# Kernel optimization log

Measured on AMD Instinct MI355X. Metric: run time of the kernel, lower is better.

## Reference

```python
import jax, jax.numpy as jnp
import numpy as np

TIMESTEPS = 1000
NOISE_LEVEL = 0.1


def setup_inputs() -> dict:
    key = jax.random.key(0)
    # images normalized to [0, 1], matching the clip range used by the model
    x = jax.random.uniform(key, (32, 512, 512, 3), dtype=jnp.float32)
    return {"x": x}


def reference(x):
    # --- forward diffusion: 1000 truly sequential add-noise + clip steps ---
    fwd_keys = jax.random.split(jax.random.key(1), TIMESTEPS)

    def fwd_step(img, k):
        noise = NOISE_LEVEL * jax.random.normal(k, img.shape, dtype=img.dtype)
        return jnp.clip(img + noise, 0.0, 1.0), None

    noisy, _ = jax.lax.scan(fwd_step, x, fwd_keys)

    # --- reverse diffusion ---
    # In the original code the reverse loop recomputes `denoised_image` from the
    # UNCHANGED `noisy_image` every iteration, so only the final iteration's
    # random draw determines the output. Mathematically equivalent single step:
    rev_key = jax.random.fold_in(jax.random.key(2), TIMESTEPS - 1)
    rev_noise = NOISE_LEVEL * jax.random.normal(rev_key, noisy.shape, dtype=noisy.dtype)
    out = jnp.clip(noisy - rev_noise, 0.0, 1.0)
    return out
```

## Files before the change

kernel.cpp:

```cpp
#include <hip/hip_runtime.h>
#include <stdint.h>


#define NTOTAL 25165824u
#define EPT    8u
#define NTHREADS (NTOTAL / EPT)
#define TS     1000

__device__ __forceinline__ void tf2x32(uint32_t k0, uint32_t k1,
                                       uint32_t x0, uint32_t x1,
                                       uint32_t& o0, uint32_t& o1) {
  const uint32_t k2 = k0 ^ k1 ^ 0x1BD11BDAu;
  x0 += k0; x1 += k1;
#define RR(r) { x0 += x1; x1 = (x1 << (r)) | (x1 >> (32 - (r))); x1 ^= x0; }
  RR(13) RR(15) RR(26) RR(6)
  x0 += k1; x1 += k2 + 1u;
  RR(17) RR(29) RR(16) RR(24)
  x0 += k2; x1 += k0 + 2u;
  RR(13) RR(15) RR(26) RR(6)
  x0 += k0; x1 += k1 + 3u;
  RR(17) RR(29) RR(16) RR(24)
  x0 += k1; x1 += k2 + 4u;
  RR(13) RR(15) RR(26) RR(6)
  x0 += k2; x1 += k0 + 5u;
#undef RR
  o0 = x0; o1 = x1;
}

__device__ __forceinline__ uint32_t tf_bits(uint32_t k0, uint32_t k1, uint32_t i) {
  uint32_t o0, o1;
  tf2x32(k0, k1, 0u, i, o0, o1);
  return o0 ^ o1;
}

__device__ __forceinline__ float bits_to_u(uint32_t b) {
  float f = __uint_as_float((b >> 9) | 0x3f800000u) - 1.0f;
  float u = fmaf(f, 2.0f, -0.99999994f);
  return fmaxf(-0.99999994f, u);
}

__device__ __forceinline__ float erfinv_f(float x) {
#pragma clang fp contract(off)
  float t = x * x;
  float m = -t;
  float u = m + 1.0f;
  float lg;
  if (u == 1.0f) {
    lg = m;
  } else {
    lg = m * __fdividef(__logf(u), u - 1.0f);
  }
  float w = -lg;
  float p;
  if (w < 5.0f) {
    w = w - 2.5f;
    p = 2.81022636e-08f;
    p = fmaf(p, w, 3.43273939e-07f);
    p = fmaf(p, w, -3.5233877e-06f);
    p = fmaf(p, w, -4.39150654e-06f);
    p = fmaf(p, w, 0.00021858087f);
    p = fmaf(p, w, -0.00125372503f);
    p = fmaf(p, w, -0.00417768164f);
    p = fmaf(p, w, 0.246640727f);
    p = fmaf(p, w, 1.50140941f);
  } else {
    w = sqrtf(w) - 3.0f;
    p = -0.000200214257f;
    p = fmaf(p, w, 0.000100950558f);
    p = fmaf(p, w, 0.00134934322f);
    p = fmaf(p, w, -0.00367342844f);
    p = fmaf(p, w, 0.00573950773f);
    p = fmaf(p, w, -0.0076224613f);
    p = fmaf(p, w, 0.00943887047f);
    p = fmaf(p, w, 1.00167406f);
    p = fmaf(p, w, 2.83297682f);
  }
  return p * x;
}

__device__ __forceinline__ float noise_from_bits(uint32_t b) {
  return 0.1f * (1.41421356f * erfinv_f(bits_to_u(b)));
}

__global__ __launch_bounds__(256) void diffusion_kernel(
    const float* __restrict__ x, float* __restrict__ out) {
  __shared__ alignas(16) uint32_t skeys[2 * TS];
  const int tid = threadIdx.x;
  for (int j = tid; j < TS; j += 256) {
    uint32_t o0, o1;
    tf2x32(0u, 1u, 0u, (uint32_t)j, o0, o1);
    skeys[2 * j] = o0;
    skeys[2 * j + 1] = o1;
  }
  __syncthreads();

  const uint32_t i = blockIdx.x * 256u + (uint32_t)tid;
  const uint32_t base = i * EPT;

  float4 v0 = ((const float4*)x)[2 * i];
  float4 v1 = ((const float4*)x)[2 * i + 1];
  float xv[EPT] = {v0.x, v0.y, v0.z, v0.w, v1.x, v1.y, v1.z, v1.w};

  for (int t = 0; t < TS; ++t) {
    const uint32_t k0 = (uint32_t)__builtin_amdgcn_readfirstlane((int)skeys[2 * t]);
    const uint32_t k1 = (uint32_t)__builtin_amdgcn_readfirstlane((int)skeys[2 * t + 1]);
    uint32_t b[EPT];
#pragma unroll
    for (uint32_t e = 0; e < EPT; ++e) b[e] = tf_bits(k0, k1, base + e);
#pragma unroll
    for (uint32_t e = 0; e < EPT; ++e) {
      xv[e] = fminf(1.0f, fmaxf(0.0f, xv[e] + noise_from_bits(b[e])));
    }
  }

  uint32_t rk0, rk1;
  tf2x32(0u, 2u, 0u, 999u, rk0, rk1);
  float ov[EPT];
#pragma unroll
  for (uint32_t e = 0; e < EPT; ++e) {
    float r = noise_from_bits(tf_bits(rk0, rk1, base + e));
    ov[e] = fminf(1.0f, fmaxf(0.0f, xv[e] - r));
  }
  float4 s0 = {ov[0], ov[1], ov[2], ov[3]};
  float4 s1 = {ov[4], ov[5], ov[6], ov[7]};
  ((float4*)out)[2 * i] = s0;
  ((float4*)out)[2 * i + 1] = s1;
}

extern "C" void kernel_launch(void* const* d_in, const int* in_sizes, int n_in,
                              void* d_out, int out_size, void* d_ws, size_t ws_size,
                              hipStream_t stream) {
  (void)in_sizes; (void)n_in; (void)d_ws; (void)ws_size; (void)out_size;
  const float* x = (const float*)d_in[0];
  float* out = (float*)d_out;
  dim3 block(256);
  dim3 grid(NTHREADS / 256);
  hipLaunchKernelGGL(diffusion_kernel, grid, block, 0, stream, x, out);
}
```

Before: 56.24 ms.

## Halve elements per thread, simplify erfinv, use alignbit rotates and med3 clamp

Cuts elements per thread from 8 to 4, which doubles the thread count to raise occupancy and latency hiding. Threefry rotates now use the alignbit builtin and the clamps use fmed3, so each costs one instruction. The erfinv log path drops the divide-based log1p correction and the u clamp, and the common branch is marked likely. Per-step keys are prefetched from LDS as uint2 one iteration ahead. The simplified log may change results slightly near zero input.

```diff
diff --git a/kernel.cpp b/kernel.cpp
--- a/kernel.cpp
+++ b/kernel.cpp
@@ -3,16 +3,20 @@
 
 
 #define NTOTAL 25165824u
-#define EPT    8u
+#define EPT    4u
 #define NTHREADS (NTOTAL / EPT)
 #define TS     1000
+
+__device__ __forceinline__ uint32_t rotl32(uint32_t x, int r) {
+  return __builtin_amdgcn_alignbit(x, x, 32 - r);
+}
 
 __device__ __forceinline__ void tf2x32(uint32_t k0, uint32_t k1,
                                        uint32_t x0, uint32_t x1,
                                        uint32_t& o0, uint32_t& o1) {
   const uint32_t k2 = k0 ^ k1 ^ 0x1BD11BDAu;
   x0 += k0; x1 += k1;
-#define RR(r) { x0 += x1; x1 = (x1 << (r)) | (x1 >> (32 - (r))); x1 ^= x0; }
+#define RR(r) { x0 += x1; x1 = rotl32(x1, r); x1 ^= x0; }
   RR(13) RR(15) RR(26) RR(6)
   x0 += k1; x1 += k2 + 1u;
   RR(17) RR(29) RR(16) RR(24)
@@ -35,96 +39,91 @@
 
 __device__ __forceinline__ float bits_to_u(uint32_t b) {
   float f = __uint_as_float((b >> 9) | 0x3f800000u) - 1.0f;
-  float u = fmaf(f, 2.0f, -0.99999994f);
-  return fmaxf(-0.99999994f, u);
+  return fmaf(f, 2.0f, -0.99999994f);
 }
 
 __device__ __forceinline__ float erfinv_f(float x) {
 #pragma clang fp contract(off)
   float t = x * x;
-  float m = -t;
-  float u = m + 1.0f;
-  float lg;
-  if (u == 1.0f) {
-    lg = m;
+  float u = 1.0f - t;
+  float w = -__logf(u);
+  float p;
+  if (__builtin_expect(!(w < 5.0f), 0)) {
+    float s = sqrtf(w) - 3.0f;
+    p = -0.000200214257f;
+    p = fmaf(p, s, 0.000100950558f);
+    p = fmaf(p, s, 0.00134934322f);
+    p = fmaf(p, s, -0.00367342844f);
+    p = fmaf(p, s, 0.00573950773f);
+    p = fmaf(p, s, -0.0076224613f);
+    p = fmaf(p, s, 0.00943887047f);
+    p = fmaf(p, s, 1.00167406f);
+    p = fmaf(p, s, 2.83297682f);
   } else {
-    lg = m * __fdividef(__logf(u), u - 1.0f);
-  }
-  float w = -lg;
-  float p;
-  if (w < 5.0f) {
-    w = w - 2.5f;
+    float s = w - 2.5f;
     p = 2.81022636e-08f;
-    p = fmaf(p, w, 3.43273939e-07f);
-    p = fmaf(p, w, -3.5233877e-06f);
-    p = fmaf(p, w, -4.39150654e-06f);
-    p = fmaf(p, w, 0.00021858087f);
-    p = fmaf(p, w, -0.00125372503f);
-    p = fmaf(p, w, -0.00417768164f);
-    p = fmaf(p, w, 0.246640727f);
-    p = fmaf(p, w, 1.50140941f);
-  } else {
-    w = sqrtf(w) - 3.0f;
-    p = -0.000200214257f;
-    p = fmaf(p, w, 0.000100950558f);
-    p = fmaf(p, w, 0.00134934322f);
-    p = fmaf(p, w, -0.00367342844f);
-    p = fmaf(p, w, 0.00573950773f);
-    p = fmaf(p, w, -0.0076224613f);
-    p = fmaf(p, w, 0.00943887047f);
-    p = fmaf(p, w, 1.00167406f);
-    p = fmaf(p, w, 2.83297682f);
+    p = fmaf(p, s, 3.43273939e-07f);
+    p = fmaf(p, s, -3.5233877e-06f);
+    p = fmaf(p, s, -4.39150654e-06f);
+    p = fmaf(p, s, 0.00021858087f);
+    p = fmaf(p, s, -0.00125372503f);
+    p = fmaf(p, s, -0.00417768164f);
+    p = fmaf(p, s, 0.246640727f);
+    p = fmaf(p, s, 1.50140941f);
   }
   return p * x;
 }
 
 __device__ __forceinline__ float noise_from_bits(uint32_t b) {
-  return 0.1f * (1.41421356f * erfinv_f(bits_to_u(b)));
+  const float c = 0.1f * 1.41421356f;
+  return c * erfinv_f(bits_to_u(b));
+}
+
+__device__ __forceinline__ float clamp01(float v) {
+  return __builtin_amdgcn_fmed3f(v, 0.0f, 1.0f);
 }
 
 __global__ __launch_bounds__(256) void diffusion_kernel(
     const float* __restrict__ x, float* __restrict__ out) {
-  __shared__ alignas(16) uint32_t skeys[2 * TS];
+  __shared__ alignas(16) uint2 skeys[TS + 1];
   const int tid = threadIdx.x;
-  for (int j = tid; j < TS; j += 256) {
+  for (int j = tid; j < TS + 1; j += 256) {
     uint32_t o0, o1;
-    tf2x32(0u, 1u, 0u, (uint32_t)j, o0, o1);
-    skeys[2 * j] = o0;
-    skeys[2 * j + 1] = o1;
+    tf2x32(0u, 1u, 0u, (uint32_t)(j < TS ? j : 0), o0, o1);
+    skeys[j] = make_uint2(o0, o1);
   }
   __syncthreads();
 
   const uint32_t i = blockIdx.x * 256u + (uint32_t)tid;
   const uint32_t base = i * EPT;
 
-  float4 v0 = ((const float4*)x)[2 * i];
-  float4 v1 = ((const float4*)x)[2 * i + 1];
-  float xv[EPT] = {v0.x, v0.y, v0.z, v0.w, v1.x, v1.y, v1.z, v1.w};
+  float4 xv = ((const float4*)x)[i];
+  float v[EPT] = {xv.x, xv.y, xv.z, xv.w};
 
+  uint2 kcur = skeys[0];
   for (int t = 0; t < TS; ++t) {
-    const uint32_t k0 = (uint32_t)__builtin_amdgcn_readfirstlane((int)skeys[2 * t]);
-    const uint32_t k1 = (uint32_t)__builtin_amdgcn_readfirstlane((int)skeys[2 * t + 1]);
+    const uint32_t k0 = (uint32_t)__builtin_amdgcn_readfirstlane((int)kcur.x);
+    const uint32_t k1 = (uint32_t)__builtin_amdgcn_readfirstlane((int)kcur.y);
+    kcur = skeys[t + 1];
     uint32_t b[EPT];
 #pragma unroll
     for (uint32_t e = 0; e < EPT; ++e) b[e] = tf_bits(k0, k1, base + e);
 #pragma unroll
     for (uint32_t e = 0; e < EPT; ++e) {
-      xv[e] = fminf(1.0f, fmaxf(0.0f, xv[e] + noise_from_bits(b[e])));
+      v[e] = clamp01(v[e] + noise_from_bits(b[e]));
     }
   }
 
   uint32_t rk0, rk1;
   tf2x32(0u, 2u, 0u, 999u, rk0, rk1);
-  float ov[EPT];
+  float4 ov;
+  float* op = &ov.x;
 #pragma unroll
   for (uint32_t e = 0; e < EPT; ++e) {
     float r = noise_from_bits(tf_bits(rk0, rk1, base + e));
-    ov[e] = fminf(1.0f, fmaxf(0.0f, xv[e] - r));
+    op[e] = clamp01(v[e] - r);
   }
-  float4 s0 = {ov[0], ov[1], ov[2], ov[3]};
-  float4 s1 = {ov[4], ov[5], ov[6], ov[7]};
-  ((float4*)out)[2 * i] = s0;
-  ((float4*)out)[2 * i + 1] = s1;
+  ((float4*)out)[i] = ov;
 }
 
 extern "C" void kernel_launch(void* const* d_in, const int* in_sizes, int n_in,
```

After: 52.03 ms. 1.08x faster.
